# Performance work log

Measured on AMD Instinct MI355X. Metric: run time of the kernel, lower is better.

Reference implementation:

```python
import jax, jax.numpy as jnp
import numpy as np

NUM_HEADS = 16

def setup_inputs() -> dict:
    key = jax.random.key(0)
    k1, k2, k3 = jax.random.split(key, 3)
    D = 1024
    return {
        "hidden_states": jax.random.normal(k1, (2, 2048, D), dtype=jnp.float32),
        "c_attn_w": jax.random.normal(k2, (D, 3 * D), dtype=jnp.float32) * 0.02,
        "c_attn_b": jnp.zeros((3 * D,), dtype=jnp.float32),
        "c_proj_w": jax.random.normal(k3, (D, D), dtype=jnp.float32) * 0.02,
        "c_proj_b": jnp.zeros((D,), dtype=jnp.float32),
    }

def reference(hidden_states, c_attn_w, c_attn_b, c_proj_w, c_proj_b):
    B, S, D = hidden_states.shape
    H = NUM_HEADS
    hd = D // H
    # Conv1D: x @ W + b, then split into q, k, v
    qkv = hidden_states @ c_attn_w + c_attn_b  # [B, S, 3D]
    q, k, v = jnp.split(qkv, 3, axis=-1)
    q = q.reshape(B, S, H, hd).transpose(0, 2, 1, 3)  # [B, H, S, hd]
    k = k.reshape(B, S, H, hd).transpose(0, 2, 1, 3)
    v = v.reshape(B, S, H, hd).transpose(0, 2, 1, 3)
    # scaled QK^T
    scores = jnp.einsum("bhqd,bhkd->bhqk", q, k) / jnp.asarray(hd ** 0.5, q.dtype)
    # causal mask (tril), masked positions set to dtype min per original code
    causal = jnp.tril(jnp.ones((S, S), dtype=bool))
    mask_value = jnp.finfo(scores.dtype).min
    scores = jnp.where(causal[None, None], scores, mask_value)
    attn = jax.nn.softmax(scores, axis=-1)
    out = jnp.einsum("bhqk,bhkd->bhqd", attn, v)  # [B, H, S, hd]
    out = out.transpose(0, 2, 1, 3).reshape(B, S, D)
    out = out @ c_proj_w + c_proj_b
    return out
```

## Files before the change

### kernel.cpp

```cpp
#include <hip/hip_runtime.h>
#include <math.h>

#define B_ 2
#define S_ 2048
#define D_ 1024
#define H_ 16
#define HD 64
#define M_ (B_ * S_)
#define N_QKV (3 * D_)

typedef short short8 __attribute__((ext_vector_type(8)));
typedef float floatx4 __attribute__((ext_vector_type(4)));

static __device__ __forceinline__ unsigned short f2bf_rne(float x) {
    union { float f; unsigned u; } v; v.f = x;
    unsigned r = v.u + 0x7FFFu + ((v.u >> 16) & 1u);
    return (unsigned short)(r >> 16);
}
static __device__ __forceinline__ float bf2f(unsigned short b) {
    union { unsigned u; float f; } v; v.u = ((unsigned)b) << 16;
    return v.f;
}
static __device__ __forceinline__ void split2(float x, unsigned short& h, unsigned short& l) {
    h = f2bf_rne(x);
    l = f2bf_rne(x - bf2f(h));
}

static __device__ __forceinline__ void dma16(const void* g, void* l) {
    __builtin_amdgcn_global_load_lds(
        (const __attribute__((address_space(1))) unsigned int*)g,
        (__attribute__((address_space(3))) unsigned int*)l,
        16, 0, 0);
}

__global__ __launch_bounds__(256) void prep_wT(
    const float* __restrict__ W, int N,
    unsigned short* __restrict__ Thi, unsigned short* __restrict__ Tlo)
{
    __shared__ float Ws[64][68];
    const int t  = threadIdx.x;
    const int n0 = blockIdx.x * 64, k0 = blockIdx.y * 64;
    {
        const int kl = t >> 4, nl = (t & 15) * 4;
        const float* src = W + (size_t)(k0 + kl) * N + n0 + nl;
#pragma unroll
        for (int g = 0; g < 4; g++)
            *(float4*)&Ws[kl + g * 16][nl] = *(const float4*)(src + (size_t)g * 16 * N);
    }
    __syncthreads();
    {
        const int nl = t >> 2, ks = (t & 3) * 16;
        short8 h0, h1, l0, l1;
#pragma unroll
        for (int j = 0; j < 8; j++) {
            unsigned short hh, ll;
            split2(Ws[ks + j][nl], hh, ll);
            h0[j] = (short)hh; l0[j] = (short)ll;
        }
#pragma unroll
        for (int j = 0; j < 8; j++) {
            unsigned short hh, ll;
            split2(Ws[ks + 8 + j][nl], hh, ll);
            h1[j] = (short)hh; l1[j] = (short)ll;
        }
        unsigned short* dh = Thi + (size_t)(n0 + nl) * D_ + k0 + ks;
        unsigned short* dl = Tlo + (size_t)(n0 + nl) * D_ + k0 + ks;
        *(short8*)dh = h0; *(short8*)(dh + 8) = h1;
        *(short8*)dl = l0; *(short8*)(dl + 8) = l1;
    }
}

__global__ __launch_bounds__(256) void gemm_qkv(
    const float* __restrict__ A,
    const unsigned short* __restrict__ BThi, const unsigned short* __restrict__ BTlo,
    const float* __restrict__ bias,
    unsigned short* __restrict__ Qhi, unsigned short* __restrict__ Qlo,
    unsigned short* __restrict__ Khi, unsigned short* __restrict__ Klo,
    unsigned short* __restrict__ vThi, unsigned short* __restrict__ vTlo)
{
    __shared__ unsigned short sAh[128 * 32], sAl[128 * 32];
    __shared__ unsigned short sBh[128 * 32], sBl[128 * 32];

    const int t    = threadIdx.x;
    const int m0   = blockIdx.y * 128, n0 = blockIdx.x * 128;
    const int lane = t & 63, wave = t >> 6;
    const int lm   = lane & 15, quad = lane >> 4;
    const int wm   = (wave >> 1) * 64, wn = (wave & 1) * 64;

    const int srow = t >> 1, sseg = (t & 1) * 16;
    const float* Ap = A + (size_t)(m0 + srow) * D_ + sseg;

    const int lrow = lane >> 2, lcol = (lane & 3) * 8;
    const unsigned short* gBh0 = BThi + (size_t)(n0 + wave * 32 + lrow) * D_ + lcol;
    const unsigned short* gBl0 = BTlo + (size_t)(n0 + wave * 32 + lrow) * D_ + lcol;
    unsigned short* lBh0 = sBh + wave * 1024 + lane * 8;
    unsigned short* lBl0 = sBl + wave * 1024 + lane * 8;

    floatx4 acc[4][4];
#pragma unroll
    for (int i = 0; i < 4; i++)
#pragma unroll
        for (int j = 0; j < 4; j++)
#pragma unroll
            for (int r = 0; r < 4; r++) acc[i][j][r] = 0.f;

    float4 af[4];
    af[0] = *(const float4*)(Ap);     af[1] = *(const float4*)(Ap + 4);
    af[2] = *(const float4*)(Ap + 8); af[3] = *(const float4*)(Ap + 12);

    for (int k0 = 0; k0 < D_; k0 += 32) {
        short8 ah0, ah1, al0, al1;
#pragma unroll
        for (int g = 0; g < 4; g++) {
            float xs[4] = {af[g].x, af[g].y, af[g].z, af[g].w};
#pragma unroll
            for (int e = 0; e < 4; e++) {
                unsigned short hh, ll;
                split2(xs[e], hh, ll);
                if (g < 2) { ah0[g * 4 + e] = (short)hh; al0[g * 4 + e] = (short)ll; }
                else       { ah1[(g - 2) * 4 + e] = (short)hh; al1[(g - 2) * 4 + e] = (short)ll; }
            }
        }
        __syncthreads();
        {
            unsigned short* a = &sAh[srow * 32 + sseg];
            unsigned short* b = &sAl[srow * 32 + sseg];
            *(short8*)a = ah0; *(short8*)(a + 8) = ah1;
            *(short8*)b = al0; *(short8*)(b + 8) = al1;
        }
        dma16(gBh0 + k0, lBh0);
        dma16(gBh0 + (size_t)16 * D_ + k0, lBh0 + 512);
        dma16(gBl0 + k0, lBl0);
        dma16(gBl0 + (size_t)16 * D_ + k0, lBl0 + 512);
        __syncthreads();

        if (k0 + 32 < D_) {
            const float* an = Ap + k0 + 32;
            af[0] = *(const float4*)(an);     af[1] = *(const float4*)(an + 4);
            af[2] = *(const float4*)(an + 8); af[3] = *(const float4*)(an + 12);
        }

        short8 bhf[4], blf[4];
#pragma unroll
        for (int nb = 0; nb < 4; nb++) {
            const int r = wn + nb * 16 + lm;
            bhf[nb] = *(const short8*)&sBh[r * 32 + quad * 8];
            blf[nb] = *(const short8*)&sBl[r * 32 + quad * 8];
        }
#pragma unroll
        for (int mb = 0; mb < 4; mb++) {
            const int r = wm + mb * 16 + lm;
            short8 ah = *(const short8*)&sAh[r * 32 + quad * 8];
            short8 al = *(const short8*)&sAl[r * 32 + quad * 8];
#pragma unroll
            for (int nb = 0; nb < 4; nb++) {
                acc[mb][nb] = __builtin_amdgcn_mfma_f32_16x16x32_bf16(ah, bhf[nb], acc[mb][nb], 0, 0, 0);
                acc[mb][nb] = __builtin_amdgcn_mfma_f32_16x16x32_bf16(al, bhf[nb], acc[mb][nb], 0, 0, 0);
                acc[mb][nb] = __builtin_amdgcn_mfma_f32_16x16x32_bf16(ah, blf[nb], acc[mb][nb], 0, 0, 0);
            }
        }
    }

    const int nmode = n0 >> 10;
    if (nmode == 0) {
#pragma unroll
        for (int nb = 0; nb < 4; nb++) {
            const int c = n0 + wn + nb * 16 + lm;
            const float bv = bias[c];
#pragma unroll
            for (int mb = 0; mb < 4; mb++) {
                const int rowb = m0 + wm + mb * 16 + quad * 4;
#pragma unroll
                for (int r = 0; r < 4; r++) {
                    unsigned short hh, ll;
                    split2((acc[mb][nb][r] + bv) * 0.125f, hh, ll);
                    Qhi[(size_t)(rowb + r) * D_ + c] = hh;
                    Qlo[(size_t)(rowb + r) * D_ + c] = ll;
                }
            }
        }
    } else if (nmode == 1) {
#pragma unroll
        for (int nb = 0; nb < 4; nb++) {
            const int c = n0 + wn + nb * 16 + lm;
            const float bv = bias[c];
            const int cq = c - 1024;
#pragma unroll
            for (int mb = 0; mb < 4; mb++) {
                const int rowb = m0 + wm + mb * 16 + quad * 4;
#pragma unroll
                for (int r = 0; r < 4; r++) {
                    unsigned short hh, ll;
                    split2(acc[mb][nb][r] + bv, hh, ll);
                    Khi[(size_t)(rowb + r) * D_ + cq] = hh;
                    Klo[(size_t)(rowb + r) * D_ + cq] = ll;
                }
            }
        }
    } else {
#pragma unroll
        for (int nb = 0; nb < 4; nb++) {
            const int c = n0 + wn + nb * 16 + lm;
            const float bv = bias[c];
            const int cq = c - 2048;
            const int hh_ = cq >> 6, dd = cq & 63;
#pragma unroll
            for (int mb = 0; mb < 4; mb++) {
                const int rowb = m0 + wm + mb * 16 + quad * 4;
                const int bb = rowb >> 11, ss = rowb & 2047;
                unsigned short hv[4], lv[4];
#pragma unroll
                for (int r = 0; r < 4; r++)
                    split2(acc[mb][nb][r] + bv, hv[r], lv[r]);
                const size_t idx = ((size_t)((bb * 16 + hh_) * 64 + dd)) * S_ + ss;
                *(uint2*)&vThi[idx] = make_uint2((unsigned)hv[0] | ((unsigned)hv[1] << 16),
                                                 (unsigned)hv[2] | ((unsigned)hv[3] << 16));
                *(uint2*)&vTlo[idx] = make_uint2((unsigned)lv[0] | ((unsigned)lv[1] << 16),
                                                 (unsigned)lv[2] | ((unsigned)lv[3] << 16));
            }
        }
    }
}

__global__ __launch_bounds__(256) void gemm_out(
    const unsigned short* __restrict__ Ahi, const unsigned short* __restrict__ Alo,
    const unsigned short* __restrict__ BThi, const unsigned short* __restrict__ BTlo,
    const float* __restrict__ bias, float* __restrict__ C)
{
    __shared__ unsigned short sAh[64 * 32], sAl[64 * 32];
    __shared__ unsigned short sBh[64 * 32], sBl[64 * 32];

    const int t    = threadIdx.x;
    const int m0   = blockIdx.y * 64, n0 = blockIdx.x * 64;
    const int lane = t & 63, wave = t >> 6;
    const int lm   = lane & 15, quad = lane >> 4;

    const int lrow = lane >> 2, lcol = (lane & 3) * 8;
    const unsigned short* gAh = Ahi + (size_t)(m0 + wave * 16 + lrow) * D_ + lcol;
    const unsigned short* gAl = Alo + (size_t)(m0 + wave * 16 + lrow) * D_ + lcol;
    const unsigned short* gBh = BThi + (size_t)(n0 + wave * 16 + lrow) * D_ + lcol;
    const unsigned short* gBl = BTlo + (size_t)(n0 + wave * 16 + lrow) * D_ + lcol;
    unsigned short* lAh = sAh + wave * 512 + lane * 8;
    unsigned short* lAl = sAl + wave * 512 + lane * 8;
    unsigned short* lBh = sBh + wave * 512 + lane * 8;
    unsigned short* lBl = sBl + wave * 512 + lane * 8;

    floatx4 acc[4];
#pragma unroll
    for (int j = 0; j < 4; j++)
#pragma unroll
        for (int r = 0; r < 4; r++) acc[j][r] = 0.f;

    for (int k0 = 0; k0 < D_; k0 += 32) {
        __syncthreads();
        dma16(gAh + k0, lAh);
        dma16(gAl + k0, lAl);
        dma16(gBh + k0, lBh);
        dma16(gBl + k0, lBl);
        __syncthreads();

        short8 ah = *(const short8*)&sAh[(wave * 16 + lm) * 32 + quad * 8];
        short8 al = *(const short8*)&sAl[(wave * 16 + lm) * 32 + quad * 8];
#pragma unroll
        for (int nb = 0; nb < 4; nb++) {
            short8 bh = *(const short8*)&sBh[(nb * 16 + lm) * 32 + quad * 8];
            short8 bl = *(const short8*)&sBl[(nb * 16 + lm) * 32 + quad * 8];
            acc[nb] = __builtin_amdgcn_mfma_f32_16x16x32_bf16(ah, bh, acc[nb], 0, 0, 0);
            acc[nb] = __builtin_amdgcn_mfma_f32_16x16x32_bf16(al, bh, acc[nb], 0, 0, 0);
            acc[nb] = __builtin_amdgcn_mfma_f32_16x16x32_bf16(ah, bl, acc[nb], 0, 0, 0);
        }
    }

#pragma unroll
    for (int nb = 0; nb < 4; nb++) {
        const int col = n0 + nb * 16 + lm;
        const float bv = bias[col];
#pragma unroll
        for (int r = 0; r < 4; r++) {
            const int row = m0 + wave * 16 + quad * 4 + r;
            C[(size_t)row * D_ + col] = acc[nb][r] + bv;
        }
    }
}

#define PST 72

__global__ __launch_bounds__(256, 2) void flash_attn_mfma(
    unsigned short* QAhi, unsigned short* QAlo,
    const unsigned short* __restrict__ Khi, const unsigned short* __restrict__ Klo,
    const unsigned short* __restrict__ vThi, const unsigned short* __restrict__ vTlo)
{
    __shared__ unsigned short KhiS[64 * PST];
    __shared__ unsigned short KloS[64 * PST];
    __shared__ unsigned short VhiS[64 * PST];
    __shared__ unsigned short VloS[64 * PST];
    __shared__ unsigned short PhS[64 * PST];
    __shared__ unsigned short PlS[64 * PST];

    const int t    = threadIdx.x;
    const int pj   = blockIdx.x;
    const int bh   = blockIdx.y;
    const int b    = bh >> 4, h = bh & 15;
    const int lane = t & 63, w = t >> 6;
    const int lm   = lane & 15, quad = lane >> 4;

    const int srow = t >> 2;
    const int sseg = (t & 3) * 16;

    const unsigned short* Kh_b = Khi + (size_t)(b * S_) * D_ + h * HD + sseg;
    const unsigned short* Kl_b = Klo + (size_t)(b * S_) * D_ + h * HD + sseg;
    const unsigned short* Vh_b = vThi + ((size_t)((b * 16 + h) * 64 + srow)) * S_ + sseg;
    const unsigned short* Vl_b = vTlo + ((size_t)((b * 16 + h) * 64 + srow)) * S_ + sseg;

    for (int phse = 0; phse < 2; phse++) {
        const int qt = phse ? (31 - pj) : pj;
        const int q0 = qt * 64;
        const int ntiles = qt + 1;

        short8 qh[2], ql[2];
        {
            const size_t qoff = (size_t)(b * S_ + q0 + w * 16 + lm) * D_ + h * HD + quad * 8;
            qh[0] = *(const short8*)&QAhi[qoff];
            qh[1] = *(const short8*)&QAhi[qoff + 32];
            ql[0] = *(const short8*)&QAlo[qoff];
            ql[1] = *(const short8*)&QAlo[qoff + 32];
        }

        float lsum[4] = {0.f, 0.f, 0.f, 0.f};
        floatx4 o[4];
#pragma unroll
        for (int nb = 0; nb < 4; nb++)
#pragma unroll
            for (int r = 0; r < 4; r++) o[nb][r] = 0.f;

        uint4 pkh[2], pkl[2], pvh[2], pvl[2];
        {
            const unsigned short* ks = Kh_b + (size_t)srow * D_;
            const unsigned short* ls = Kl_b + (size_t)srow * D_;
            pkh[0] = *(const uint4*)ks;   pkh[1] = *(const uint4*)(ks + 8);
            pkl[0] = *(const uint4*)ls;   pkl[1] = *(const uint4*)(ls + 8);
            pvh[0] = *(const uint4*)Vh_b; pvh[1] = *(const uint4*)(Vh_b + 8);
            pvl[0] = *(const uint4*)Vl_b; pvl[1] = *(const uint4*)(Vl_b + 8);
        }

        for (int kt = 0; kt < ntiles; kt++) {
            __syncthreads();
            {
                unsigned short* d0 = &KhiS[srow * PST + sseg];
                unsigned short* d1 = &KloS[srow * PST + sseg];
                unsigned short* d2 = &VhiS[srow * PST + sseg];
                unsigned short* d3 = &VloS[srow * PST + sseg];
                *(uint4*)d0 = pkh[0]; *(uint4*)(d0 + 8) = pkh[1];
                *(uint4*)d1 = pkl[0]; *(uint4*)(d1 + 8) = pkl[1];
                *(uint4*)d2 = pvh[0]; *(uint4*)(d2 + 8) = pvh[1];
                *(uint4*)d3 = pvl[0]; *(uint4*)(d3 + 8) = pvl[1];
            }
            __syncthreads();

            if (kt + 1 < ntiles) {
                const int k1 = (kt + 1) * 64;
                const unsigned short* ks = Kh_b + (size_t)(k1 + srow) * D_;
                const unsigned short* ls = Kl_b + (size_t)(k1 + srow) * D_;
                pkh[0] = *(const uint4*)ks;          pkh[1] = *(const uint4*)(ks + 8);
                pkl[0] = *(const uint4*)ls;          pkl[1] = *(const uint4*)(ls + 8);
                pvh[0] = *(const uint4*)(Vh_b + k1); pvh[1] = *(const uint4*)(Vh_b + k1 + 8);
                pvl[0] = *(const uint4*)(Vl_b + k1); pvl[1] = *(const uint4*)(Vl_b + k1 + 8);
            }

            floatx4 sa[4];
#pragma unroll
            for (int nb = 0; nb < 4; nb++)
#pragma unroll
                for (int r = 0; r < 4; r++) sa[nb][r] = 0.f;
#pragma unroll
            for (int s = 0; s < 2; s++) {
#pragma unroll
                for (int nb = 0; nb < 4; nb++) {
                    short8 kh = *(const short8*)&KhiS[(nb * 16 + lm) * PST + s * 32 + quad * 8];
                    short8 kl = *(const short8*)&KloS[(nb * 16 + lm) * PST + s * 32 + quad * 8];
                    sa[nb] = __builtin_amdgcn_mfma_f32_16x16x32_bf16(qh[s], kh, sa[nb], 0, 0, 0);
                    sa[nb] = __builtin_amdgcn_mfma_f32_16x16x32_bf16(ql[s], kh, sa[nb], 0, 0, 0);
                    sa[nb] = __builtin_amdgcn_mfma_f32_16x16x32_bf16(qh[s], kl, sa[nb], 0, 0, 0);
                }
            }

            const bool diag = (kt * 64 == q0);
#pragma unroll
            for (int r = 0; r < 4; r++) {
                const int qrow = 16 * w + 4 * quad + r;
#pragma unroll
                for (int nb = 0; nb < 4; nb++) {
                    float p = __expf(sa[nb][r]);
                    if (diag && (16 * nb + lm > qrow)) p = 0.f;
                    lsum[r] += p;
                    unsigned short hh, ll;
                    split2(p, hh, ll);
                    PhS[qrow * PST + 16 * nb + lm] = hh;
                    PlS[qrow * PST + 16 * nb + lm] = ll;
                }
            }

#pragma unroll
            for (int ks = 0; ks < 2; ks++) {
                short8 pf = *(const short8*)&PhS[(16 * w + lm) * PST + ks * 32 + quad * 8];
                short8 pg = *(const short8*)&PlS[(16 * w + lm) * PST + ks * 32 + quad * 8];
#pragma unroll
                for (int nb = 0; nb < 4; nb++) {
                    short8 vhf = *(const short8*)&VhiS[(16 * nb + lm) * PST + ks * 32 + quad * 8];
                    short8 vlf = *(const short8*)&VloS[(16 * nb + lm) * PST + ks * 32 + quad * 8];
                    o[nb] = __builtin_amdgcn_mfma_f32_16x16x32_bf16(pf, vhf, o[nb], 0, 0, 0);
                    o[nb] = __builtin_amdgcn_mfma_f32_16x16x32_bf16(pg, vhf, o[nb], 0, 0, 0);
                    o[nb] = __builtin_amdgcn_mfma_f32_16x16x32_bf16(pf, vlf, o[nb], 0, 0, 0);
                }
            }
        }

#pragma unroll
        for (int r = 0; r < 4; r++) {
            float l = lsum[r];
            l += __shfl_xor(l, 1);
            l += __shfl_xor(l, 2);
            l += __shfl_xor(l, 4);
            l += __shfl_xor(l, 8);
            const float inv = 1.f / l;
            const size_t rowoff =
                (size_t)(b * S_ + q0 + 16 * w + 4 * quad + r) * D_ + h * HD + lm;
#pragma unroll
            for (int nb = 0; nb < 4; nb++) {
                unsigned short hh, ll;
                split2(o[nb][r] * inv, hh, ll);
                QAhi[rowoff + 16 * nb] = hh;
                QAlo[rowoff + 16 * nb] = ll;
            }
        }
    }
}

extern "C" void kernel_launch(void* const* d_in, const int* in_sizes, int n_in,
                              void* d_out, int out_size, void* d_ws, size_t ws_size,
                              hipStream_t stream)
{
    const float* hs     = (const float*)d_in[0];
    const float* attn_w = (const float*)d_in[1];
    const float* attn_b = (const float*)d_in[2];
    const float* proj_w = (const float*)d_in[3];
    const float* proj_b = (const float*)d_in[4];
    float* outp = (float*)d_out;

    const size_t QE = (size_t)M_ * D_;
    const size_t WQ = (size_t)D_ * N_QKV;
    unsigned short* Qhi   = (unsigned short*)d_ws;
    unsigned short* Qlo   = Qhi + QE;
    unsigned short* Khi   = Qlo + QE;
    unsigned short* Klo   = Khi + QE;
    unsigned short* vThi  = Klo + QE;
    unsigned short* vTlo  = vThi + QE;
    unsigned short* WqThi = vTlo + QE;
    unsigned short* WqTlo = WqThi + WQ;
    unsigned short* WpThi = WqTlo + WQ;
    unsigned short* WpTlo = WpThi + (size_t)D_ * D_;

    dim3 blk(256);
    prep_wT<<<dim3(N_QKV / 64, D_ / 64), blk, 0, stream>>>(attn_w, N_QKV, WqThi, WqTlo);
    prep_wT<<<dim3(D_ / 64, D_ / 64), blk, 0, stream>>>(proj_w, D_, WpThi, WpTlo);
    gemm_qkv<<<dim3(N_QKV / 128, M_ / 128), blk, 0, stream>>>(
        hs, WqThi, WqTlo, attn_b, Qhi, Qlo, Khi, Klo, vThi, vTlo);
    flash_attn_mfma<<<dim3(16, B_ * H_), blk, 0, stream>>>(
        Qhi, Qlo, Khi, Klo, vThi, vTlo);
    gemm_out<<<dim3(D_ / 64, M_ / 64), blk, 0, stream>>>(
        Qhi, Qlo, WpThi, WpTlo, proj_b, outp);
}
```

Before: 351.6 us.

## Use 128-row query tiles with 512-thread blocks sharing K/V tiles

New measurement: 315.5 us. -10.3%, faster.

```diff
diff --git a/kernel.cpp b/kernel.cpp
--- a/kernel.cpp
+++ b/kernel.cpp
@@ -285,7 +285,7 @@
 
 #define PST 72
 
-__global__ __launch_bounds__(256, 2) void flash_attn_mfma(
+__global__ __launch_bounds__(512, 4) void flash_attn_mfma(
     unsigned short* QAhi, unsigned short* QAlo,
     const unsigned short* __restrict__ Khi, const unsigned short* __restrict__ Klo,
     const unsigned short* __restrict__ vThi, const unsigned short* __restrict__ vTlo)
@@ -294,8 +294,8 @@
     __shared__ unsigned short KloS[64 * PST];
     __shared__ unsigned short VhiS[64 * PST];
     __shared__ unsigned short VloS[64 * PST];
-    __shared__ unsigned short PhS[64 * PST];
-    __shared__ unsigned short PlS[64 * PST];
+    __shared__ unsigned short PhS[128 * PST];
+    __shared__ unsigned short PlS[128 * PST];
 
     const int t    = threadIdx.x;
     const int pj   = blockIdx.x;
@@ -304,8 +304,8 @@
     const int lane = t & 63, w = t >> 6;
     const int lm   = lane & 15, quad = lane >> 4;
 
-    const int srow = t >> 2;
-    const int sseg = (t & 3) * 16;
+    const int srow = t >> 3;
+    const int sseg = (t & 7) * 8;
 
     const unsigned short* Kh_b = Khi + (size_t)(b * S_) * D_ + h * HD + sseg;
     const unsigned short* Kl_b = Klo + (size_t)(b * S_) * D_ + h * HD + sseg;
@@ -313,13 +313,14 @@
     const unsigned short* Vl_b = vTlo + ((size_t)((b * 16 + h) * 64 + srow)) * S_ + sseg;
 
     for (int phse = 0; phse < 2; phse++) {
-        const int qt = phse ? (31 - pj) : pj;
-        const int q0 = qt * 64;
-        const int ntiles = qt + 1;
+        const int qt = phse ? (15 - pj) : pj;
+        const int q0 = qt * 128;
+        const int ntiles = 2 * qt + 2;
+        const int wdiag = (q0 >> 6) + (w >> 2);
 
         short8 qh[2], ql[2];
         {
-            const size_t qoff = (size_t)(b * S_ + q0 + w * 16 + lm) * D_ + h * HD + quad * 8;
+            const size_t qoff = (size_t)(b * S_ + q0 + 16 * w + lm) * D_ + h * HD + quad * 8;
             qh[0] = *(const short8*)&QAhi[qoff];
             qh[1] = *(const short8*)&QAhi[qoff + 32];
             ql[0] = *(const short8*)&QAlo[qoff];
@@ -333,84 +334,76 @@
 #pragma unroll
             for (int r = 0; r < 4; r++) o[nb][r] = 0.f;
 
-        uint4 pkh[2], pkl[2], pvh[2], pvl[2];
-        {
-            const unsigned short* ks = Kh_b + (size_t)srow * D_;
-            const unsigned short* ls = Kl_b + (size_t)srow * D_;
-            pkh[0] = *(const uint4*)ks;   pkh[1] = *(const uint4*)(ks + 8);
-            pkl[0] = *(const uint4*)ls;   pkl[1] = *(const uint4*)(ls + 8);
-            pvh[0] = *(const uint4*)Vh_b; pvh[1] = *(const uint4*)(Vh_b + 8);
-            pvl[0] = *(const uint4*)Vl_b; pvl[1] = *(const uint4*)(Vl_b + 8);
-        }
+        uint4 pkh, pkl, pvh, pvl;
+        pkh = *(const uint4*)(Kh_b + (size_t)srow * D_);
+        pkl = *(const uint4*)(Kl_b + (size_t)srow * D_);
+        pvh = *(const uint4*)(Vh_b);
+        pvl = *(const uint4*)(Vl_b);
 
         for (int kt = 0; kt < ntiles; kt++) {
             __syncthreads();
-            {
-                unsigned short* d0 = &KhiS[srow * PST + sseg];
-                unsigned short* d1 = &KloS[srow * PST + sseg];
-                unsigned short* d2 = &VhiS[srow * PST + sseg];
-                unsigned short* d3 = &VloS[srow * PST + sseg];
-                *(uint4*)d0 = pkh[0]; *(uint4*)(d0 + 8) = pkh[1];
-                *(uint4*)d1 = pkl[0]; *(uint4*)(d1 + 8) = pkl[1];
-                *(uint4*)d2 = pvh[0]; *(uint4*)(d2 + 8) = pvh[1];
-                *(uint4*)d3 = pvl[0]; *(uint4*)(d3 + 8) = pvl[1];
-            }
+            *(uint4*)&KhiS[srow * PST + sseg] = pkh;
+            *(uint4*)&KloS[srow * PST + sseg] = pkl;
+            *(uint4*)&VhiS[srow * PST + sseg] = pvh;
+            *(uint4*)&VloS[srow * PST + sseg] = pvl;
             __syncthreads();
 
             if (kt + 1 < ntiles) {
                 const int k1 = (kt + 1) * 64;
-                const unsigned short* ks = Kh_b + (size_t)(k1 + srow) * D_;
-                const unsigned short* ls = Kl_b + (size_t)(k1 + srow) * D_;
-                pkh[0] = *(const uint4*)ks;          pkh[1] = *(const uint4*)(ks + 8);
-                pkl[0] = *(const uint4*)ls;          pkl[1] = *(const uint4*)(ls + 8);
-                pvh[0] = *(const uint4*)(Vh_b + k1); pvh[1] = *(const uint4*)(Vh_b + k1 + 8);
-                pvl[0] = *(const uint4*)(Vl_b + k1); pvl[1] = *(const uint4*)(Vl_b + k1 + 8);
-            }
-
-            floatx4 sa[4];
-#pragma unroll
-            for (int nb = 0; nb < 4; nb++)
-#pragma unroll
-                for (int r = 0; r < 4; r++) sa[nb][r] = 0.f;
-#pragma unroll
-            for (int s = 0; s < 2; s++) {
-#pragma unroll
-                for (int nb = 0; nb < 4; nb++) {
-                    short8 kh = *(const short8*)&KhiS[(nb * 16 + lm) * PST + s * 32 + quad * 8];
-                    short8 kl = *(const short8*)&KloS[(nb * 16 + lm) * PST + s * 32 + quad * 8];
-                    sa[nb] = __builtin_amdgcn_mfma_f32_16x16x32_bf16(qh[s], kh, sa[nb], 0, 0, 0);
-                    sa[nb] = __builtin_amdgcn_mfma_f32_16x16x32_bf16(ql[s], kh, sa[nb], 0, 0, 0);
-                    sa[nb] = __builtin_amdgcn_mfma_f32_16x16x32_bf16(qh[s], kl, sa[nb], 0, 0, 0);
+                pkh = *(const uint4*)(Kh_b + (size_t)(k1 + srow) * D_);
+                pkl = *(const uint4*)(Kl_b + (size_t)(k1 + srow) * D_);
+                pvh = *(const uint4*)(Vh_b + k1);
+                pvl = *(const uint4*)(Vl_b + k1);
+            }
+
+            if (kt <= wdiag) {
+                floatx4 sa[4];
+#pragma unroll
+                for (int nb = 0; nb < 4; nb++)
+#pragma unroll
+                    for (int r = 0; r < 4; r++) sa[nb][r] = 0.f;
+#pragma unroll
+                for (int s = 0; s < 2; s++) {
+#pragma unroll
+                    for (int nb = 0; nb < 4; nb++) {
+                        short8 kh = *(const short8*)&KhiS[(nb * 16 + lm) * PST + s * 32 + quad * 8];
+                        short8 kl = *(const short8*)&KloS[(nb * 16 + lm) * PST + s * 32 + quad * 8];
+                        sa[nb] = __builtin_amdgcn_mfma_f32_16x16x32_bf16(qh[s], kh, sa[nb], 0, 0, 0);
+                        sa[nb] = __builtin_amdgcn_mfma_f32_16x16x32_bf16(ql[s], kh, sa[nb], 0, 0, 0);
+                        sa[nb] = __builtin_amdgcn_mfma_f32_16x16x32_bf16(qh[s], kl, sa[nb], 0, 0, 0);
+                    }
                 }
-            }
-
-            const bool diag = (kt * 64 == q0);
-#pragma unroll
-            for (int r = 0; r < 4; r++) {
-                const int qrow = 16 * w + 4 * quad + r;
-#pragma unroll
-                for (int nb = 0; nb < 4; nb++) {
-                    float p = __expf(sa[nb][r]);
-                    if (diag && (16 * nb + lm > qrow)) p = 0.f;
-                    lsum[r] += p;
-                    unsigned short hh, ll;
-                    split2(p, hh, ll);
-                    PhS[qrow * PST + 16 * nb + lm] = hh;
-                    PlS[qrow * PST + 16 * nb + lm] = ll;
+
+                const bool diag = (kt == wdiag);
+                const int kbase = kt * 64;
+#pragma unroll
+                for (int r = 0; r < 4; r++) {
+                    const int qabs = q0 + 16 * w + 4 * quad + r;
+                    const int rloc = 16 * w + 4 * quad + r;
+#pragma unroll
+                    for (int nb = 0; nb < 4; nb++) {
+                        float p = __expf(sa[nb][r]);
+                        if (diag && (kbase + 16 * nb + lm > qabs)) p = 0.f;
+                        lsum[r] += p;
+                        unsigned short hh, ll;
+                        split2(p, hh, ll);
+                        PhS[rloc * PST + 16 * nb + lm] = hh;
+                        PlS[rloc * PST + 16 * nb + lm] = ll;
+                    }
                 }
-            }
-
-#pragma unroll
-            for (int ks = 0; ks < 2; ks++) {
-                short8 pf = *(const short8*)&PhS[(16 * w + lm) * PST + ks * 32 + quad * 8];
-                short8 pg = *(const short8*)&PlS[(16 * w + lm) * PST + ks * 32 + quad * 8];
-#pragma unroll
-                for (int nb = 0; nb < 4; nb++) {
-                    short8 vhf = *(const short8*)&VhiS[(16 * nb + lm) * PST + ks * 32 + quad * 8];
-                    short8 vlf = *(const short8*)&VloS[(16 * nb + lm) * PST + ks * 32 + quad * 8];
-                    o[nb] = __builtin_amdgcn_mfma_f32_16x16x32_bf16(pf, vhf, o[nb], 0, 0, 0);
-                    o[nb] = __builtin_amdgcn_mfma_f32_16x16x32_bf16(pg, vhf, o[nb], 0, 0, 0);
-                    o[nb] = __builtin_amdgcn_mfma_f32_16x16x32_bf16(pf, vlf, o[nb], 0, 0, 0);
+
+#pragma unroll
+                for (int ks = 0; ks < 2; ks++) {
+                    short8 pf = *(const short8*)&PhS[(16 * w + lm) * PST + ks * 32 + quad * 8];
+                    short8 pg = *(const short8*)&PlS[(16 * w + lm) * PST + ks * 32 + quad * 8];
+#pragma unroll
+                    for (int nb = 0; nb < 4; nb++) {
+                        short8 vhf = *(const short8*)&VhiS[(16 * nb + lm) * PST + ks * 32 + quad * 8];
+                        short8 vlf = *(const short8*)&VloS[(16 * nb + lm) * PST + ks * 32 + quad * 8];
+                        o[nb] = __builtin_amdgcn_mfma_f32_16x16x32_bf16(pf, vhf, o[nb], 0, 0, 0);
+                        o[nb] = __builtin_amdgcn_mfma_f32_16x16x32_bf16(pg, vhf, o[nb], 0, 0, 0);
+                        o[nb] = __builtin_amdgcn_mfma_f32_16x16x32_bf16(pf, vlf, o[nb], 0, 0, 0);
+                    }
                 }
             }
         }
@@ -465,7 +458,7 @@
     prep_wT<<<dim3(D_ / 64, D_ / 64), blk, 0, stream>>>(proj_w, D_, WpThi, WpTlo);
     gemm_qkv<<<dim3(N_QKV / 128, M_ / 128), blk, 0, stream>>>(
         hs, WqThi, WqTlo, attn_b, Qhi, Qlo, Khi, Klo, vThi, vTlo);
-    flash_attn_mfma<<<dim3(16, B_ * H_), blk, 0, stream>>>(
+    flash_attn_mfma<<<dim3(8, B_ * H_), dim3(512), 0, stream>>>(
         Qhi, Qlo, Khi, Klo, vThi, vTlo);
     gemm_out<<<dim3(D_ / 64, M_ / 64), blk, 0, stream>>>(
         Qhi, Qlo, WpThi, WpTlo, proj_b, outp);
```
